# Kernel optimization log

Measured on AMD Instinct MI355X. Metric: run time of the kernel, lower is better.

Reference implementation:

```python
import jax, jax.numpy as jnp
import numpy as np

N_NODES = 50000
N_EDGES = 800000
IN_DIM = 128
HIDDEN = 64
NEG_SLOPE = 0.2


def setup_inputs() -> dict:
    key = jax.random.key(0)
    ks = jax.random.split(key, 8)
    x = jax.random.normal(ks[0], (N_NODES, IN_DIM), dtype=jnp.float32)
    edge_index = jax.random.randint(ks[1], (2, N_EDGES), 0, N_NODES, dtype=jnp.int64)
    # GATConv params (heads=1)
    W = jax.random.normal(ks[2], (HIDDEN, IN_DIM), dtype=jnp.float32) / np.sqrt(IN_DIM)
    att_src = jax.random.normal(ks[3], (HIDDEN,), dtype=jnp.float32) / np.sqrt(HIDDEN)
    att_dst = jax.random.normal(ks[4], (HIDDEN,), dtype=jnp.float32) / np.sqrt(HIDDEN)
    bias_conv = jnp.zeros((HIDDEN,), dtype=jnp.float32)
    # final Linear(hidden, 1)
    W_lin = jax.random.normal(ks[5], (1, HIDDEN), dtype=jnp.float32) / np.sqrt(HIDDEN)
    b_lin = jnp.zeros((1,), dtype=jnp.float32)
    return {"x": x, "edge_index": edge_index, "W": W, "att_src": att_src,
            "att_dst": att_dst, "bias_conv": bias_conv, "W_lin": W_lin, "b_lin": b_lin}


def _gat_forward(x, edge_index, W, att_src, att_dst, bias_conv, W_lin, b_lin):
    n = x.shape[0]
    # add self-loops (PyG GATConv default)
    loop = jnp.arange(n, dtype=edge_index.dtype)
    src = jnp.concatenate([edge_index[0], loop])  # source nodes j (messages from)
    dst = jnp.concatenate([edge_index[1], loop])  # destination nodes i (aggregated at)

    h = x @ W.T                                   # [N, H] projected features
    a_src = h @ att_src                           # [N]
    a_dst = h @ att_dst                           # [N]

    e = jax.nn.leaky_relu(a_src[src] + a_dst[dst], NEG_SLOPE)  # [E']
    # segment softmax over incoming edges of each destination node
    m = jax.ops.segment_max(e, dst, num_segments=n)            # [N]
    ex = jnp.exp(e - m[dst])
    s = jax.ops.segment_sum(ex, dst, num_segments=n)           # [N]
    alpha = ex / s[dst]                                        # [E']

    out = jax.ops.segment_sum(alpha[:, None] * h[src], dst, num_segments=n)
    out = out + bias_conv                         # [N, H]

    out = jax.nn.relu(out)
    # dropout p=0.5 is a no-op in eval mode
    y = jax.nn.sigmoid(out @ W_lin.T + b_lin)     # [N, 1]
    return y


def reference(x, edge_index, W, att_src, att_dst, bias_conv, W_lin, b_lin):
    return _gat_forward(x, edge_index, W, att_src, att_dst, bias_conv, W_lin, b_lin)
```

## Files before the change

kernel.cpp:

```cpp
#include <hip/hip_runtime.h>
#include <hip/hip_bf16.h>
#include <hip/hip_fp16.h>
#include <cstdint>

#define IND 128
#define HID 64
#define NEG_SLOPE 0.2f
#define EPB 4096
#define CBSHIFT 8
#define BCAP 8192

__device__ __forceinline__ unsigned short f2bf_bits(float f) {
  __hip_bfloat16 b = __float2bfloat16(f);
  return *reinterpret_cast<unsigned short*>(&b);
}
__device__ __forceinline__ unsigned short f2h_bits(float f) {
  __half h = __float2half(f);
  return *reinterpret_cast<unsigned short*>(&h);
}
__device__ __forceinline__ float h2f_bits(unsigned short u) {
  __half_raw r; r.x = u;
  return __half2float(__half(r));
}
__device__ __forceinline__ float bf2f_bits(unsigned short u) {
  return __uint_as_float((unsigned)u << 16);
}
__device__ __forceinline__ unsigned pack_bf2(float lo, float hi) {
  return (unsigned)f2bf_bits(lo) | ((unsigned)f2bf_bits(hi) << 16);
}
__device__ __forceinline__ float bf_lo(unsigned u) {
  return __uint_as_float(u << 16);
}
__device__ __forceinline__ float bf_hi(unsigned u) {
  return __uint_as_float(u & 0xFFFF0000u);
}

__global__ __launch_bounds__(256) void k_proj(
    const float* __restrict__ x, const float* __restrict__ W,
    const float* __restrict__ att_s, const float* __restrict__ att_d,
    unsigned short* __restrict__ h, float* __restrict__ a_src,
    float* __restrict__ a_dst, int* __restrict__ gcur, int nbuck, int n)
{
  __shared__ float    xs[64 * 128];
  __shared__ unsigned wt[64 * 64];
  __shared__ float sa_l[64], sd_l[64];

  const int tid = threadIdx.x;
  const int nodeBase = blockIdx.x * 64;

  if (blockIdx.x == 0 && tid < nbuck) gcur[tid] = 0;
  if (tid < 64) { sa_l[tid] = 0.f; sd_l[tid] = 0.f; }

#pragma unroll
  for (int it = 0; it < 4; ++it) {
    int fi = (it * 256 + tid) * 8;
    int row = fi >> 7, k = fi & 127;
    float4 w0 = *(const float4*)(W + fi);
    float4 w1 = *(const float4*)(W + fi + 4);
    uint4 pv;
    pv.x = pack_bf2(w0.x, w0.y);
    pv.y = pack_bf2(w0.z, w0.w);
    pv.z = pack_bf2(w1.x, w1.y);
    pv.w = pack_bf2(w1.z, w1.w);
    int c = (k >> 3) ^ ((row >> 2) & 7);
    ((uint4*)wt)[row * 16 + c] = pv;
  }
#pragma unroll
  for (int it = 0; it < 8; ++it) {
    int fi = (it * 256 + tid) * 4;
    int nl = fi >> 7, k = fi & 127;
    int ks = k ^ (((nl >> 2) & 7) << 2);
    int node = nodeBase + nl; if (node >= n) node = n - 1;
    float4 v = *(const float4*)(x + (size_t)node * IND + k);
    *(float4*)&xs[nl * 128 + ks] = v;
  }
  __syncthreads();

  const int ng = tid & 15;
  const int hg = tid >> 4;
  const int swzA = (ng & 7) << 2;
  const int swzB = hg & 7;
  const float* xrow0 = &xs[(4 * ng) * 128];
  const uint4* wrow0 = ((const uint4*)wt) + (4 * hg) * 16;

  float acc[4][4];
#pragma unroll
  for (int j = 0; j < 4; ++j)
#pragma unroll
    for (int i = 0; i < 4; ++i) acc[j][i] = 0.f;

  for (int k = 0; k < IND; k += 8) {
    float4 a0[4], a1[4];
#pragma unroll
    for (int j = 0; j < 4; ++j) {
      a0[j] = *(const float4*)(xrow0 + j * 128 + (k ^ swzA));
      a1[j] = *(const float4*)(xrow0 + j * 128 + ((k + 4) ^ swzA));
    }
    uint4 bw[4];
#pragma unroll
    for (int i = 0; i < 4; ++i)
      bw[i] = wrow0[i * 16 + ((k >> 3) ^ swzB)];

#pragma unroll
    for (int i = 0; i < 4; ++i) {
      float b0 = bf_lo(bw[i].x), b1 = bf_hi(bw[i].x);
      float b2 = bf_lo(bw[i].y), b3 = bf_hi(bw[i].y);
      float b4 = bf_lo(bw[i].z), b5 = bf_hi(bw[i].z);
      float b6 = bf_lo(bw[i].w), b7 = bf_hi(bw[i].w);
#pragma unroll
      for (int j = 0; j < 4; ++j) {
        acc[j][i] = fmaf(a0[j].x, b0, acc[j][i]);
        acc[j][i] = fmaf(a0[j].y, b1, acc[j][i]);
        acc[j][i] = fmaf(a0[j].z, b2, acc[j][i]);
        acc[j][i] = fmaf(a0[j].w, b3, acc[j][i]);
        acc[j][i] = fmaf(a1[j].x, b4, acc[j][i]);
        acc[j][i] = fmaf(a1[j].y, b5, acc[j][i]);
        acc[j][i] = fmaf(a1[j].z, b6, acc[j][i]);
        acc[j][i] = fmaf(a1[j].w, b7, acc[j][i]);
      }
    }
  }

#pragma unroll
  for (int j = 0; j < 4; ++j) {
    int node = nodeBase + 4 * ng + j;
    if (node < n) {
      ushort4 hv;
      hv.x = f2bf_bits(acc[j][0]);
      hv.y = f2bf_bits(acc[j][1]);
      hv.z = f2bf_bits(acc[j][2]);
      hv.w = f2bf_bits(acc[j][3]);
      *(ushort4*)(h + (size_t)node * HID + 4 * hg) = hv;
    }
  }

  float4 as4 = *(const float4*)(att_s + 4 * hg);
  float4 ad4 = *(const float4*)(att_d + 4 * hg);
#pragma unroll
  for (int j = 0; j < 4; ++j) {
    float ps = acc[j][0]*as4.x + acc[j][1]*as4.y + acc[j][2]*as4.z + acc[j][3]*as4.w;
    float pd = acc[j][0]*ad4.x + acc[j][1]*ad4.y + acc[j][2]*ad4.z + acc[j][3]*ad4.w;
    ps += __shfl_xor(ps, 16, 64); ps += __shfl_xor(ps, 32, 64);
    pd += __shfl_xor(pd, 16, 64); pd += __shfl_xor(pd, 32, 64);
    if ((tid & 63) < 16) {
      atomicAdd(&sa_l[4 * ng + j], ps);
      atomicAdd(&sd_l[4 * ng + j], pd);
    }
  }
  __syncthreads();
  if (tid < 64) {
    int node = nodeBase + tid;
    if (node < n) { a_src[node] = sa_l[tid]; a_dst[node] = sd_l[tid]; }
  }
}

__global__ __launch_bounds__(1024) void k_sortout(
    const int* __restrict__ ei, int* __restrict__ gcur,
    unsigned* __restrict__ tmp, int E, long long E2, int nbuck)
{
  __shared__ int hist[256];
  __shared__ int sums[256];
  __shared__ int cur[256];
  __shared__ int gbase[256];
  __shared__ unsigned sorted[EPB];

  const int tid = threadIdx.x;
  if (tid < 256) hist[tid] = 0;
  __syncthreads();

  const long long i0 = (long long)blockIdx.x * EPB;

  unsigned pk[EPB / 1024];
#pragma unroll
  for (int j = 0; j < EPB / 1024; ++j) {
    long long idx = i0 + j * 1024 + tid;
    unsigned v = 0xFFFFFFFFu;
    if (idx < E2) {
      int s, d;
      if (idx < E) { s = ei[idx]; d = ei[E + idx]; }
      else         { s = d = (int)(idx - E); }
      v = ((unsigned)d << 16) | (unsigned)s;
      atomicAdd(&hist[d >> CBSHIFT], 1);
    }
    pk[j] = v;
  }
  __syncthreads();

  if (tid < 256) sums[tid] = hist[tid];
  __syncthreads();
  for (int off = 1; off < 256; off <<= 1) {
    int t = (tid >= off && tid < 256) ? sums[tid - off] : 0;
    __syncthreads();
    if (tid < 256) sums[tid] += t;
    __syncthreads();
  }
  if (tid < 256) {
    const int lstart_t = sums[tid] - hist[tid];
    cur[tid] = lstart_t;
    gbase[tid] = (tid < nbuck && hist[tid] > 0)
                   ? tid * BCAP + atomicAdd(&gcur[tid], hist[tid]) : 0;
  }
  __syncthreads();
  if (tid < 256) hist[tid] = sums[tid] - hist[tid];
  __syncthreads();

#pragma unroll
  for (int j = 0; j < EPB / 1024; ++j) {
    unsigned v = pk[j];
    if (v != 0xFFFFFFFFu) {
      int b = v >> (16 + CBSHIFT);
      int lpos = atomicAdd(&cur[b], 1);
      sorted[lpos] = v;
    }
  }
  __syncthreads();

  const int cntE = (int)((E2 - i0 < EPB) ? (E2 - i0) : EPB);
  for (int i = tid; i < cntE; i += 1024) {
    unsigned v = sorted[i];
    int b = v >> (16 + CBSHIFT);
    tmp[gbase[b] + (i - hist[b])] = v;
  }
}

__global__ __launch_bounds__(1024) void k_csr(
    const unsigned* __restrict__ tmp, const int* __restrict__ gcur,
    const float* __restrict__ a_src, const float* __restrict__ a_dst,
    int* __restrict__ row_start, int* __restrict__ deg_out,
    unsigned* __restrict__ csr4, int n, int nbuck)
{
  __shared__ int degl[256], sums[256], cur[256];
  __shared__ float adl[256];

  const int tid = threadIdx.x;
  const int b   = blockIdx.x;
  const int n0  = b << CBSHIFT;
  const int base = b * BCAP;
  const int next = base + gcur[b];

  if (tid < 256) {
    degl[tid] = 0;
    const int node = n0 + tid;
    adl[tid] = (node < n) ? a_dst[node] : 0.f;
  }
  __syncthreads();

  for (int i = base + tid; i < next; i += 1024)
    atomicAdd(&degl[(tmp[i] >> 16) - n0], 1);
  __syncthreads();

  if (tid < 256) sums[tid] = degl[tid];
  __syncthreads();
  for (int off = 1; off < 256; off <<= 1) {
    int t = (tid >= off && tid < 256) ? sums[tid - off] : 0;
    __syncthreads();
    if (tid < 256) sums[tid] += t;
    __syncthreads();
  }
  if (tid < 256) {
    const int rs = base + sums[tid] - degl[tid];
    cur[tid] = rs;
    const int node = n0 + tid;
    if (node < n) { row_start[node] = rs; deg_out[node] = degl[tid]; }
  }
  __syncthreads();

  for (int i = base + tid; i < next; i += 1024) {
    unsigned v = tmp[i];
    int s  = (int)(v & 0xFFFFu);
    int dl = (int)(v >> 16) - n0;
    float sc = a_src[s] + adl[dl];
    sc = (sc >= 0.f) ? sc : NEG_SLOPE * sc;
    float w = expf(sc);
    int pos = atomicAdd(&cur[dl], 1);
    csr4[pos] = (unsigned)s | ((unsigned)f2h_bits(w) << 16);
  }
}

__global__ __launch_bounds__(256) void k_gather_final(
    const int* __restrict__ row_start, const int* __restrict__ deg,
    const unsigned* __restrict__ csr4, const unsigned short* __restrict__ h,
    const float* __restrict__ bias, const float* __restrict__ W_lin,
    const float* __restrict__ b_lin, float* __restrict__ y, int n)
{
  const int lane = threadIdx.x & 63;
  const int wid  = threadIdx.x >> 6;
  const int node = blockIdx.x * 4 + wid;
  if (node >= n) return;

  const int rs = row_start[node];
  const int dg = deg[node];

  const int quarter = lane >> 4;
  const int sub     = lane & 15;

  float wpart = 0.f;
  float acc0 = 0.f, acc1 = 0.f, acc2 = 0.f, acc3 = 0.f;

  for (int b = 0; b < dg; b += 64) {
    int i = b + lane;
    unsigned pk = (i < dg) ? csr4[rs + i] : 0u;
    wpart += h2f_bits((unsigned short)(pk >> 16));
    const int cnt = (dg - b < 64) ? (dg - b) : 64;

    int j = 0;
    for (; j + 8 <= cnt; j += 8) {
#pragma unroll
      for (int g = 0; g < 2; ++g) {
        int e = j + 4 * g + quarter;
        unsigned pe = __shfl(pk, e, 64);
        float we = h2f_bits((unsigned short)(pe >> 16));
        unsigned se = pe & 0xFFFFu;
        ushort4 hb = ((const ushort4*)(h + (size_t)se * HID))[sub];
        acc0 = fmaf(we, bf2f_bits(hb.x), acc0);
        acc1 = fmaf(we, bf2f_bits(hb.y), acc1);
        acc2 = fmaf(we, bf2f_bits(hb.z), acc2);
        acc3 = fmaf(we, bf2f_bits(hb.w), acc3);
      }
    }
    for (; j < cnt; j += 4) {
      int e = j + quarter;
      bool val = e < cnt;
      unsigned pe = __shfl(pk, val ? e : 0, 64);
      float we = val ? h2f_bits((unsigned short)(pe >> 16)) : 0.f;
      unsigned se = val ? (pe & 0xFFFFu) : 0u;
      ushort4 hb = ((const ushort4*)(h + (size_t)se * HID))[sub];
      acc0 = fmaf(we, bf2f_bits(hb.x), acc0);
      acc1 = fmaf(we, bf2f_bits(hb.y), acc1);
      acc2 = fmaf(we, bf2f_bits(hb.z), acc2);
      acc3 = fmaf(we, bf2f_bits(hb.w), acc3);
    }
  }

  acc0 += __shfl_xor(acc0, 16, 64); acc0 += __shfl_xor(acc0, 32, 64);
  acc1 += __shfl_xor(acc1, 16, 64); acc1 += __shfl_xor(acc1, 32, 64);
  acc2 += __shfl_xor(acc2, 16, 64); acc2 += __shfl_xor(acc2, 32, 64);
  acc3 += __shfl_xor(acc3, 16, 64); acc3 += __shfl_xor(acc3, 32, 64);

  float wsum = wpart;
#pragma unroll
  for (int o = 32; o; o >>= 1) wsum += __shfl_xor(wsum, o, 64);
  const float inv = 1.f / wsum;

  float4 bb = ((const float4*)bias)[sub];
  float4 ww = ((const float4*)W_lin)[sub];
  float v0 = fmaxf(acc0 * inv + bb.x, 0.f);
  float v1 = fmaxf(acc1 * inv + bb.y, 0.f);
  float v2 = fmaxf(acc2 * inv + bb.z, 0.f);
  float v3 = fmaxf(acc3 * inv + bb.w, 0.f);
  float z = v0 * ww.x + v1 * ww.y + v2 * ww.z + v3 * ww.w;
#pragma unroll
  for (int o = 8; o; o >>= 1) z += __shfl_xor(z, o, 64);
  if (lane == 0)
    y[node] = 1.f / (1.f + expf(-(z + b_lin[0])));
}


extern "C" void kernel_launch(void* const* d_in, const int* in_sizes, int n_in,
                              void* d_out, int out_size, void* d_ws, size_t ws_size,
                              hipStream_t stream)
{
  const float* x     = (const float*)d_in[0];
  const int*   ei    = (const int*)d_in[1];
  const float* W     = (const float*)d_in[2];
  const float* att_s = (const float*)d_in[3];
  const float* att_d = (const float*)d_in[4];
  const float* bias  = (const float*)d_in[5];
  const float* W_lin = (const float*)d_in[6];
  const float* b_lin = (const float*)d_in[7];
  float* y = (float*)d_out;

  const int n = in_sizes[0] / IND;
  const int E = in_sizes[1] / 2;
  const long long E2 = (long long)E + n;
  const int nblk  = (int)((E2 + EPB - 1) / EPB);
  const int nbuck = (n + (1 << CBSHIFT) - 1) >> CBSHIFT;

  char* ws = (char*)d_ws;
  unsigned short* h = (unsigned short*)ws; ws += (size_t)n * HID * sizeof(unsigned short);
  float*    a_src  = (float*)ws;    ws += (size_t)n * sizeof(float);
  float*    a_dst  = (float*)ws;    ws += (size_t)n * sizeof(float);
  int*      row_st = (int*)ws;      ws += (size_t)n * sizeof(int);
  int*      deg    = (int*)ws;      ws += (size_t)n * sizeof(int);
  int*      gcur   = (int*)ws;      ws += (size_t)nbuck * sizeof(int);
  unsigned* tmp    = (unsigned*)ws; ws += (size_t)nbuck * BCAP * sizeof(unsigned);
  unsigned* csr4   = (unsigned*)ws; ws += (size_t)nbuck * BCAP * sizeof(unsigned);

  k_proj<<<(n + 63) / 64, 256, 0, stream>>>(x, W, att_s, att_d, h, a_src, a_dst,
                                            gcur, nbuck, n);

  k_sortout<<<nblk, 1024, 0, stream>>>(ei, gcur, tmp, E, E2, nbuck);
  k_csr<<<nbuck, 1024, 0, stream>>>(tmp, gcur, a_src, a_dst, row_st, deg, csr4,
                                    n, nbuck);

  k_gather_final<<<(n + 3) / 4, 256, 0, stream>>>(
      row_st, deg, csr4, h, bias, W_lin, b_lin, y, n);
}
```

Before: 147.6 us.

## Fuse projection and edge bucket-sort into one launch with block-role dispatch

Merges the node projection kernel and the edge bucketing kernel into a single launch where the first blocks sort edges and the rest do the projection, sharing one shared-memory buffer. The sort part drops from 1024 to 256 threads per block, and the gcur zeroing moves to a hipMemsetAsync. The intent is to remove a kernel boundary and let the two independent stages run concurrently on the GPU. The cost is an extra memset launch, fewer sort threads per block, and shared-memory use sized for the larger role, which may lower occupancy.

```diff
diff --git a/kernel.cpp b/kernel.cpp
--- a/kernel.cpp
+++ b/kernel.cpp
@@ -9,6 +9,8 @@
 #define EPB 4096
 #define CBSHIFT 8
 #define BCAP 8192
+#define SORT_THREADS 256
+#define EPT (EPB / SORT_THREADS)
 
 __device__ __forceinline__ unsigned short f2bf_bits(float f) {
   __hip_bfloat16 b = __float2bfloat16(f);
@@ -35,20 +37,91 @@
   return __uint_as_float(u & 0xFFFF0000u);
 }
 
-__global__ __launch_bounds__(256) void k_proj(
+__global__ __launch_bounds__(256) void k_proj_sort(
     const float* __restrict__ x, const float* __restrict__ W,
     const float* __restrict__ att_s, const float* __restrict__ att_d,
     unsigned short* __restrict__ h, float* __restrict__ a_src,
-    float* __restrict__ a_dst, int* __restrict__ gcur, int nbuck, int n)
+    float* __restrict__ a_dst,
+    const int* __restrict__ ei, int* __restrict__ gcur,
+    unsigned* __restrict__ tmp, int E, long long E2,
+    int nSort, int nbuck, int n)
 {
-  __shared__ float    xs[64 * 128];
-  __shared__ unsigned wt[64 * 64];
-  __shared__ float sa_l[64], sd_l[64];
-
+  __shared__ __align__(16) char smem[49664];
   const int tid = threadIdx.x;
-  const int nodeBase = blockIdx.x * 64;
-
-  if (blockIdx.x == 0 && tid < nbuck) gcur[tid] = 0;
+
+  if (blockIdx.x < (unsigned)nSort) {
+    int* hist       = (int*)smem;
+    int* sums       = hist + 256;
+    int* cur        = sums + 256;
+    int* gbase      = cur + 256;
+    unsigned* sorted = (unsigned*)(gbase + 256);
+
+    hist[tid] = 0;
+    __syncthreads();
+
+    const long long i0 = (long long)blockIdx.x * EPB;
+
+    unsigned pk[EPT];
+#pragma unroll
+    for (int j = 0; j < EPT; ++j) {
+      long long idx = i0 + j * SORT_THREADS + tid;
+      unsigned v = 0xFFFFFFFFu;
+      if (idx < E2) {
+        int s, d;
+        if (idx < E) { s = ei[idx]; d = ei[E + idx]; }
+        else         { s = d = (int)(idx - E); }
+        v = ((unsigned)d << 16) | (unsigned)s;
+        atomicAdd(&hist[d >> CBSHIFT], 1);
+      }
+      pk[j] = v;
+    }
+    __syncthreads();
+
+    sums[tid] = hist[tid];
+    __syncthreads();
+    for (int off = 1; off < 256; off <<= 1) {
+      int t = (tid >= off) ? sums[tid - off] : 0;
+      __syncthreads();
+      sums[tid] += t;
+      __syncthreads();
+    }
+    {
+      const int lstart_t = sums[tid] - hist[tid];
+      cur[tid] = lstart_t;
+      gbase[tid] = (tid < nbuck && hist[tid] > 0)
+                     ? tid * BCAP + atomicAdd(&gcur[tid], hist[tid]) : 0;
+    }
+    __syncthreads();
+    hist[tid] = sums[tid] - hist[tid];
+    __syncthreads();
+
+#pragma unroll
+    for (int j = 0; j < EPT; ++j) {
+      unsigned v = pk[j];
+      if (v != 0xFFFFFFFFu) {
+        int b = v >> (16 + CBSHIFT);
+        int lpos = atomicAdd(&cur[b], 1);
+        sorted[lpos] = v;
+      }
+    }
+    __syncthreads();
+
+    const int cntE = (int)((E2 - i0 < EPB) ? (E2 - i0) : EPB);
+    for (int i = tid; i < cntE; i += SORT_THREADS) {
+      unsigned v = sorted[i];
+      int b = v >> (16 + CBSHIFT);
+      tmp[gbase[b] + (i - hist[b])] = v;
+    }
+    return;
+  }
+
+  float*    xs   = (float*)smem;
+  unsigned* wt   = (unsigned*)(smem + 32768);
+  float*    sa_l = (float*)(smem + 49152);
+  float*    sd_l = (float*)(smem + 49408);
+
+  const int nodeBase = (blockIdx.x - nSort) * 64;
+
   if (tid < 64) { sa_l[tid] = 0.f; sd_l[tid] = 0.f; }
 
 #pragma unroll
@@ -151,75 +224,6 @@
   if (tid < 64) {
     int node = nodeBase + tid;
     if (node < n) { a_src[node] = sa_l[tid]; a_dst[node] = sd_l[tid]; }
-  }
-}
-
-__global__ __launch_bounds__(1024) void k_sortout(
-    const int* __restrict__ ei, int* __restrict__ gcur,
-    unsigned* __restrict__ tmp, int E, long long E2, int nbuck)
-{
-  __shared__ int hist[256];
-  __shared__ int sums[256];
-  __shared__ int cur[256];
-  __shared__ int gbase[256];
-  __shared__ unsigned sorted[EPB];
-
-  const int tid = threadIdx.x;
-  if (tid < 256) hist[tid] = 0;
-  __syncthreads();
-
-  const long long i0 = (long long)blockIdx.x * EPB;
-
-  unsigned pk[EPB / 1024];
-#pragma unroll
-  for (int j = 0; j < EPB / 1024; ++j) {
-    long long idx = i0 + j * 1024 + tid;
-    unsigned v = 0xFFFFFFFFu;
-    if (idx < E2) {
-      int s, d;
-      if (idx < E) { s = ei[idx]; d = ei[E + idx]; }
-      else         { s = d = (int)(idx - E); }
-      v = ((unsigned)d << 16) | (unsigned)s;
-      atomicAdd(&hist[d >> CBSHIFT], 1);
-    }
-    pk[j] = v;
-  }
-  __syncthreads();
-
-  if (tid < 256) sums[tid] = hist[tid];
-  __syncthreads();
-  for (int off = 1; off < 256; off <<= 1) {
-    int t = (tid >= off && tid < 256) ? sums[tid - off] : 0;
-    __syncthreads();
-    if (tid < 256) sums[tid] += t;
-    __syncthreads();
-  }
-  if (tid < 256) {
-    const int lstart_t = sums[tid] - hist[tid];
-    cur[tid] = lstart_t;
-    gbase[tid] = (tid < nbuck && hist[tid] > 0)
-                   ? tid * BCAP + atomicAdd(&gcur[tid], hist[tid]) : 0;
-  }
-  __syncthreads();
-  if (tid < 256) hist[tid] = sums[tid] - hist[tid];
-  __syncthreads();
-
-#pragma unroll
-  for (int j = 0; j < EPB / 1024; ++j) {
-    unsigned v = pk[j];
-    if (v != 0xFFFFFFFFu) {
-      int b = v >> (16 + CBSHIFT);
-      int lpos = atomicAdd(&cur[b], 1);
-      sorted[lpos] = v;
-    }
-  }
-  __syncthreads();
-
-  const int cntE = (int)((E2 - i0 < EPB) ? (E2 - i0) : EPB);
-  for (int i = tid; i < cntE; i += 1024) {
-    unsigned v = sorted[i];
-    int b = v >> (16 + CBSHIFT);
-    tmp[gbase[b] + (i - hist[b])] = v;
   }
 }
 
@@ -373,7 +377,8 @@
   const int n = in_sizes[0] / IND;
   const int E = in_sizes[1] / 2;
   const long long E2 = (long long)E + n;
-  const int nblk  = (int)((E2 + EPB - 1) / EPB);
+  const int nSort = (int)((E2 + EPB - 1) / EPB);
+  const int nProj = (n + 63) / 64;
   const int nbuck = (n + (1 << CBSHIFT) - 1) >> CBSHIFT;
 
   char* ws = (char*)d_ws;
@@ -386,10 +391,12 @@
   unsigned* tmp    = (unsigned*)ws; ws += (size_t)nbuck * BCAP * sizeof(unsigned);
   unsigned* csr4   = (unsigned*)ws; ws += (size_t)nbuck * BCAP * sizeof(unsigned);
 
-  k_proj<<<(n + 63) / 64, 256, 0, stream>>>(x, W, att_s, att_d, h, a_src, a_dst,
-                                            gcur, nbuck, n);
-
-  k_sortout<<<nblk, 1024, 0, stream>>>(ei, gcur, tmp, E, E2, nbuck);
+  hipMemsetAsync(gcur, 0, (size_t)nbuck * sizeof(int), stream);
+
+  k_proj_sort<<<nSort + nProj, 256, 0, stream>>>(
+      x, W, att_s, att_d, h, a_src, a_dst,
+      ei, gcur, tmp, E, E2, nSort, nbuck, n);
+
   k_csr<<<nbuck, 1024, 0, stream>>>(tmp, gcur, a_src, a_dst, row_st, deg, csr4,
                                     n, nbuck);
 
```

After: 141.0 us. 1.05x faster.
